# Kernel optimization log

Hardware: AMD Instinct MI355X
Metric: run time of the kernel (lower is better)

Reference implementation:

```python
import jax, jax.numpy as jnp
import numpy as np

B, NF, FD = 2048, 64, 32   # batch, n_features, feature_dim
S = NF // 2                # n_sites
D, OD = 32, 32             # bond_dim, out_dim


def setup_inputs() -> dict:
    key = jax.random.key(0)
    k1, k2, k3, k4 = jax.random.split(key, 4)
    sc = 1.0 / np.sqrt(FD * D)
    x = jax.random.normal(k1, (B, NF, FD), dtype=jnp.float32)
    L = jax.random.normal(k2, (S, FD, D, D), dtype=jnp.float32) * sc
    R = jax.random.normal(k3, (S, FD, D, D), dtype=jnp.float32) * sc
    O = jax.random.normal(k4, (S, D, D, OD), dtype=jnp.float32) * sc
    bias = jnp.zeros((S, OD), dtype=jnp.float32)
    return {"x": x, "L": L, "R": R, "O": O, "bias": bias}


def reference(x, L, R, O, bias):
    # x: [B, 2*S, FD] -> left/right features per site
    xL = x[:, 0::2, :]  # [B, S, FD]
    xR = x[:, 1::2, :]  # [B, S, FD]
    # feature -> bond matrices
    A = jnp.einsum('bsf,sfam->bsam', xL, L)   # [B, S, D, D]
    Bm = jnp.einsum('bsg,sgan->bsan', xR, R)  # [B, S, D, D]
    # contract shared bond leg a, then output tensor
    M = jnp.einsum('bsam,bsan->bsmn', A, Bm)  # [B, S, D, D]
    out = jnp.einsum('bsmn,smno->bso', M, O)  # [B, S, OD]
    return out + bias  # bias broadcast over batch; activation is None
```

## Files before the change

### kernel.cpp

```cpp
#include <hip/hip_runtime.h>
#include <hip/hip_bf16.h>

typedef __attribute__((ext_vector_type(4)))  _Float16 h4;
typedef __attribute__((ext_vector_type(8)))  _Float16 h8;
typedef __attribute__((ext_vector_type(4)))  float f32x4;
typedef __attribute__((ext_vector_type(16))) float f32x16;

__device__ __forceinline__ int sdecode(int sp) { return ((sp & 7) << 2) | (sp >> 3); }

__global__ __launch_bounds__(64) void conv_kernel(
    const float* __restrict__ Rg, const float* __restrict__ Og,
    _Float16* __restrict__ Rb, char* __restrict__ Opp)
{
    __shared__ float tile[32][33];
    const int bid = blockIdx.x;
    const int s = sdecode(bid & 31), q = (bid >> 5) & 31, which = bid >> 10;
    const int t = threadIdx.x, tl = t & 31, th = t >> 5;

    if (which == 0) {
        #pragma unroll
        for (int j = 0; j < 16; ++j) {
            int ar = 2*j + th;
            tile[tl][ar] = Rg[(((size_t)s*32 + q)*32 + ar)*32 + tl];
        }
        __syncthreads();
        _Float16* dst = Rb + ((size_t)s*32 + q)*1024;
        #pragma unroll
        for (int it = 0; it < 4; ++it) {
            int nr = it*8 + (t >> 3), a0 = (t & 7)*4;
            h4 w;
            #pragma unroll
            for (int k = 0; k < 4; ++k) w[k] = (_Float16)tile[nr][a0 + k];
            *(h4*)(dst + nr*32 + a0) = w;
        }
    } else {
        #pragma unroll
        for (int j = 0; j < 16; ++j) {
            int nr = 2*j + th;
            tile[tl][nr] = Og[(((size_t)s*32 + q)*32 + nr)*32 + tl];
        }
        __syncthreads();
        char* dst = Opp + (size_t)s*65536 + q*2048;
        int o = t & 31, cq = t >> 5;
        #pragma unroll
        for (int it = 0; it < 2; ++it) {
            int c = it*2 + cq;
            h8 w;
            #pragma unroll
            for (int k = 0; k < 8; ++k) w[k] = (_Float16)tile[o][c*8 + k];
            *(h8*)(dst + c*512 + o*16) = w;
        }
    }
}

__global__ __launch_bounds__(256, 2) void tmake_kernel(
    const float* __restrict__ Lg, const _Float16* __restrict__ Rb,
    const char* __restrict__ Opp, char* __restrict__ Tp)
{
    __shared__ __align__(16) char Wl[65536];
    const int bid = blockIdx.x;
    const int s = sdecode(bid & 31), f = bid >> 5;
    const int t = threadIdx.x, wid = t >> 6, l = t & 63;
    const int llo = l & 15, lhi = l >> 4;

    const float* Lsf = Lg + ((size_t)s*32 + f)*1024;
    h8 bfr[2];
    #pragma unroll
    for (int mt = 0; mt < 2; ++mt)
        #pragma unroll
        for (int j = 0; j < 8; ++j)
            bfr[mt][j] = (_Float16)Lsf[(8*lhi + j)*32 + mt*16 + llo];

    const _Float16* Rbs = Rb + (size_t)s*32768;

    #pragma unroll 4
    for (int nt = 0; nt < 16; ++nt) {
        int gnb = (wid*16 + nt)*16;
        h8 af = *(const h8*)(Rbs + (gnb + llo)*32 + 8*lhi);
        int g = gnb >> 5;
        int nbase = (gnb & 31) + 4*lhi;
        #pragma unroll
        for (int mt = 0; mt < 2; ++mt) {
            f32x4 d = __builtin_amdgcn_mfma_f32_16x16x32_f16(af, bfr[mt], (f32x4)(0.f), 0, 0, 0);
            int m = mt*16 + llo;
            h4 w;
            #pragma unroll
            for (int r = 0; r < 4; ++r) w[r] = (_Float16)d[r];
            int byte = (g*2048 + m*64 + nbase*2) ^ ((((g & 7) ^ (m & 7))) << 4);
            *(h4*)(Wl + byte) = w;
        }
    }
    __syncthreads();

    const int ot = wid & 1, kq = wid >> 1;
    const int orow = ot*16 + llo;
    const char* Opps = Opp + (size_t)s*65536;
    f32x4 acc0 = (f32x4)(0.f), acc1 = (f32x4)(0.f);
    #pragma unroll 4
    for (int ksl = 0; ksl < 16; ++ksl) {
        int ks = kq*16 + ksl;
        h8 bf = *(const h8*)(Opps + (ks*4 + lhi)*512 + orow*16);
        {
            int grow = llo;
            int byte = (grow*2048 + ks*64 + lhi*16) ^ ((((grow & 7) ^ (ks & 7))) << 4);
            h8 af = *(const h8*)(Wl + byte);
            acc0 = __builtin_amdgcn_mfma_f32_16x16x32_f16(af, bf, acc0, 0, 0, 0);
        }
        {
            int grow = 16 + llo;
            int byte = (grow*2048 + ks*64 + lhi*16) ^ ((((grow & 7) ^ (ks & 7))) << 4);
            h8 af = *(const h8*)(Wl + byte);
            acc1 = __builtin_amdgcn_mfma_f32_16x16x32_f16(af, bf, acc1, 0, 0, 0);
        }
    }
    __syncthreads();
    if (kq == 1) {
        *(f32x4*)(Wl + ((ot*2 + 0)*64 + l)*16) = acc0;
        *(f32x4*)(Wl + ((ot*2 + 1)*64 + l)*16) = acc1;
    }
    __syncthreads();
    if (kq == 0) {
        acc0 += *(const f32x4*)(Wl + ((ot*2 + 0)*64 + l)*16);
        acc1 += *(const f32x4*)(Wl + ((ot*2 + 1)*64 + l)*16);
        char* Tps = Tp + (size_t)s*65536;
        h4 w0, w1;
        #pragma unroll
        for (int r = 0; r < 4; ++r) { w0[r] = (_Float16)acc0[r]; w1[r] = (_Float16)acc1[r]; }
        *(h4*)(Tps + (f*2 + 0)*1024 + orow*32 + lhi*8) = w0;
        *(h4*)(Tps + (f*2 + 1)*1024 + orow*32 + lhi*8) = w1;
    }
}

__global__ __launch_bounds__(256, 2) void main_kernel(
    const float* __restrict__ x, const char* __restrict__ Tp,
    const float* __restrict__ bias, float* __restrict__ out)
{
    __shared__ __align__(16) char Tl[65536];

    const int bid = blockIdx.x;
    const int s = sdecode(bid & 31);
    const int b0 = (bid >> 5) * 128;
    const int t = threadIdx.x, wid = t >> 6, l = t & 63;
    const int lo5 = l & 31, hi = l >> 5;

    const char* Tps = Tp + (size_t)s*65536;

    uint4 tv[8];
    #pragma unroll
    for (int i = 0; i < 8; ++i)
        tv[i] = *(const uint4*)(Tps + (i*256 + t)*16);

    const float* xrow = x + (size_t)(b0 + wid*32 + lo5)*2048 + s*64;
    float4 xlv[8];
    #pragma unroll
    for (int i = 0; i < 8; ++i) xlv[i] = *(const float4*)(xrow + i*4);
    const float* xrp = xrow + 32 + hi*8;
    float4 xr00 = *(const float4*)(xrp);
    float4 xr01 = *(const float4*)(xrp + 4);
    float4 xr10 = *(const float4*)(xrp + 16);
    float4 xr11 = *(const float4*)(xrp + 20);

    #pragma unroll
    for (int i = 0; i < 8; ++i)
        *(uint4*)(Tl + (i*256 + t)*16) = tv[i];
    #pragma unroll
    for (int i = 0; i < 8; ++i)
        tv[i] = *(const uint4*)(Tps + ((i + 8)*256 + t)*16);

    h4 xlh[8];
    #pragma unroll
    for (int i = 0; i < 8; ++i) {
        xlh[i][0] = (_Float16)xlv[i].x; xlh[i][1] = (_Float16)xlv[i].y;
        xlh[i][2] = (_Float16)xlv[i].z; xlh[i][3] = (_Float16)xlv[i].w;
    }
    h8 xr_a, xr_b;
    xr_a[0] = (_Float16)xr00.x; xr_a[1] = (_Float16)xr00.y;
    xr_a[2] = (_Float16)xr00.z; xr_a[3] = (_Float16)xr00.w;
    xr_a[4] = (_Float16)xr01.x; xr_a[5] = (_Float16)xr01.y;
    xr_a[6] = (_Float16)xr01.z; xr_a[7] = (_Float16)xr01.w;
    xr_b[0] = (_Float16)xr10.x; xr_b[1] = (_Float16)xr10.y;
    xr_b[2] = (_Float16)xr10.z; xr_b[3] = (_Float16)xr10.w;
    xr_b[4] = (_Float16)xr11.x; xr_b[5] = (_Float16)xr11.y;
    xr_b[6] = (_Float16)xr11.z; xr_b[7] = (_Float16)xr11.w;

    #pragma unroll
    for (int i = 0; i < 8; ++i)
        *(uint4*)(Tl + ((i + 8)*256 + t)*16) = tv[i];
    __syncthreads();

    f32x16 acc_e = (f32x16)(0.f), acc_o = (f32x16)(0.f);
    #pragma unroll
    for (int ksl = 0; ksl < 64; ++ksl) {
        h8 bf = *(const h8*)(Tl + ksl*1024 + lo5*32 + hi*16);
        _Float16 xs = xlh[ksl >> 3][(ksl >> 1) & 3];
        if (ksl & 1) {
            h8 z = xr_b * xs;
            acc_o = __builtin_amdgcn_mfma_f32_32x32x16_f16(z, bf, acc_o, 0, 0, 0);
        } else {
            h8 z = xr_a * xs;
            acc_e = __builtin_amdgcn_mfma_f32_32x32x16_f16(z, bf, acc_e, 0, 0, 0);
        }
    }
    f32x16 acc = acc_e + acc_o;

    __syncthreads();
    #pragma unroll
    for (int r = 0; r < 16; ++r) {
        int row = (r & 3) + 8*(r >> 2) + 4*hi;
        *(float*)(Tl + wid*4096 + row*128 + lo5*4) = acc[r];
    }
    __syncthreads();

    const float* bias_s = bias + s*32;
    #pragma unroll
    for (int i = 0; i < 4; ++i) {
        int u = i*256 + t;
        int row = u >> 3, colq = u & 7;
        f32x4 v = *(const f32x4*)(Tl + u*16);
        f32x4 bv = *(const f32x4*)(bias_s + colq*4);
        *(f32x4*)(out + (size_t)(b0 + row)*1024 + s*32 + colq*4) = v + bv;
    }
}

extern "C" void kernel_launch(void* const* d_in, const int* in_sizes, int n_in,
                              void* d_out, int out_size, void* d_ws, size_t ws_size,
                              hipStream_t stream) {
    const float* x    = (const float*)d_in[0];
    const float* L    = (const float*)d_in[1];
    const float* R    = (const float*)d_in[2];
    const float* O    = (const float*)d_in[3];
    const float* bias = (const float*)d_in[4];
    float* out = (float*)d_out;

    _Float16* Rb  = (_Float16*)d_ws;
    char*     Opp = (char*)d_ws + 2097152;
    char*     Tp  = (char*)d_ws + 4194304;

    conv_kernel<<<dim3(2048), 64, 0, stream>>>(R, O, Rb, Opp);
    tmake_kernel<<<dim3(1024), 256, 0, stream>>>(L, Rb, Opp, Tp);
    main_kernel<<<dim3(512), 256, 0, stream>>>(x, Tp, bias, out);
}
```

Before: 28.90 us.

## Stream T fragments from global into register ring, drop LDS staging in main kernel

```diff
diff --git a/kernel.cpp b/kernel.cpp
--- a/kernel.cpp
+++ b/kernel.cpp
@@ -131,26 +131,20 @@
     }
 }
 
-__global__ __launch_bounds__(256, 2) void main_kernel(
+__global__ __launch_bounds__(64, 4) void main_kernel(
     const float* __restrict__ x, const char* __restrict__ Tp,
     const float* __restrict__ bias, float* __restrict__ out)
 {
-    __shared__ __align__(16) char Tl[65536];
-
     const int bid = blockIdx.x;
-    const int s = sdecode(bid & 31);
-    const int b0 = (bid >> 5) * 128;
-    const int t = threadIdx.x, wid = t >> 6, l = t & 63;
-    const int lo5 = l & 31, hi = l >> 5;
+    const int s = bid & 31;
+    const int b0 = (bid >> 5) * 32;
+    const int t = threadIdx.x;
+    const int lo5 = t & 31, hi = t >> 5;
 
     const char* Tps = Tp + (size_t)s*65536;
-
-    uint4 tv[8];
-    #pragma unroll
-    for (int i = 0; i < 8; ++i)
-        tv[i] = *(const uint4*)(Tps + (i*256 + t)*16);
-
-    const float* xrow = x + (size_t)(b0 + wid*32 + lo5)*2048 + s*64;
+    const char* Tbase = Tps + lo5*32 + hi*16;
+
+    const float* xrow = x + (size_t)(b0 + lo5)*2048 + s*64;
     float4 xlv[8];
     #pragma unroll
     for (int i = 0; i < 8; ++i) xlv[i] = *(const float4*)(xrow + i*4);
@@ -160,12 +154,10 @@
     float4 xr10 = *(const float4*)(xrp + 16);
     float4 xr11 = *(const float4*)(xrp + 20);
 
+    h8 ring[8];
     #pragma unroll
     for (int i = 0; i < 8; ++i)
-        *(uint4*)(Tl + (i*256 + t)*16) = tv[i];
-    #pragma unroll
-    for (int i = 0; i < 8; ++i)
-        tv[i] = *(const uint4*)(Tps + ((i + 8)*256 + t)*16);
+        ring[i] = *(const h8*)(Tbase + i*1024);
 
     h4 xlh[8];
     #pragma unroll
@@ -183,15 +175,12 @@
     xr_b[4] = (_Float16)xr11.x; xr_b[5] = (_Float16)xr11.y;
     xr_b[6] = (_Float16)xr11.z; xr_b[7] = (_Float16)xr11.w;
 
-    #pragma unroll
-    for (int i = 0; i < 8; ++i)
-        *(uint4*)(Tl + ((i + 8)*256 + t)*16) = tv[i];
-    __syncthreads();
-
     f32x16 acc_e = (f32x16)(0.f), acc_o = (f32x16)(0.f);
     #pragma unroll
     for (int ksl = 0; ksl < 64; ++ksl) {
-        h8 bf = *(const h8*)(Tl + ksl*1024 + lo5*32 + hi*16);
+        h8 bf = ring[ksl & 7];
+        if (ksl < 56)
+            ring[ksl & 7] = *(const h8*)(Tbase + (ksl + 8)*1024);
         _Float16 xs = xlh[ksl >> 3][(ksl >> 1) & 3];
         if (ksl & 1) {
             h8 z = xr_b * xs;
@@ -203,22 +192,11 @@
     }
     f32x16 acc = acc_e + acc_o;
 
-    __syncthreads();
+    const float bv = bias[s*32 + lo5];
     #pragma unroll
     for (int r = 0; r < 16; ++r) {
         int row = (r & 3) + 8*(r >> 2) + 4*hi;
-        *(float*)(Tl + wid*4096 + row*128 + lo5*4) = acc[r];
-    }
-    __syncthreads();
-
-    const float* bias_s = bias + s*32;
-    #pragma unroll
-    for (int i = 0; i < 4; ++i) {
-        int u = i*256 + t;
-        int row = u >> 3, colq = u & 7;
-        f32x4 v = *(const f32x4*)(Tl + u*16);
-        f32x4 bv = *(const f32x4*)(bias_s + colq*4);
-        *(f32x4*)(out + (size_t)(b0 + row)*1024 + s*32 + colq*4) = v + bv;
+        out[(size_t)(b0 + row)*1024 + s*32 + lo5] = acc[r] + bv;
     }
 }
 
@@ -238,5 +216,5 @@
 
     conv_kernel<<<dim3(2048), 64, 0, stream>>>(R, O, Rb, Opp);
     tmake_kernel<<<dim3(1024), 256, 0, stream>>>(L, Rb, Opp, Tp);
-    main_kernel<<<dim3(512), 256, 0, stream>>>(x, Tp, bias, out);
-}
+    main_kernel<<<dim3(2048), 64, 0, stream>>>(x, Tp, bias, out);
+}
```

Result: slower. 37.77 us (+30.7%).

## Fuse three kernels into one persistent kernel with per-site global barriers

Applied to the files above, without the earlier changes.

```diff
diff --git a/kernel.cpp b/kernel.cpp
--- a/kernel.cpp
+++ b/kernel.cpp
@@ -5,152 +5,159 @@
 typedef __attribute__((ext_vector_type(8)))  _Float16 h8;
 typedef __attribute__((ext_vector_type(4)))  float f32x4;
 typedef __attribute__((ext_vector_type(16))) float f32x16;
+typedef __attribute__((ext_vector_type(4)))  unsigned int u32x4;
 
 __device__ __forceinline__ int sdecode(int sp) { return ((sp & 7) << 2) | (sp >> 3); }
 
-__global__ __launch_bounds__(64) void conv_kernel(
+__global__ __launch_bounds__(256, 2) void fused_kernel(
+    const float* __restrict__ x, const float* __restrict__ Lg,
     const float* __restrict__ Rg, const float* __restrict__ Og,
-    _Float16* __restrict__ Rb, char* __restrict__ Opp)
+    const float* __restrict__ bias, float* __restrict__ out,
+    _Float16* __restrict__ Rb, char* __restrict__ Opp, char* __restrict__ Tp,
+    unsigned* __restrict__ bar)
 {
-    __shared__ float tile[32][33];
+    __shared__ __align__(16) char smem[65536];
+
     const int bid = blockIdx.x;
-    const int s = sdecode(bid & 31), q = (bid >> 5) & 31, which = bid >> 10;
-    const int t = threadIdx.x, tl = t & 31, th = t >> 5;
-
-    if (which == 0) {
-        #pragma unroll
-        for (int j = 0; j < 16; ++j) {
-            int ar = 2*j + th;
-            tile[tl][ar] = Rg[(((size_t)s*32 + q)*32 + ar)*32 + tl];
-        }
-        __syncthreads();
-        _Float16* dst = Rb + ((size_t)s*32 + q)*1024;
-        #pragma unroll
-        for (int it = 0; it < 4; ++it) {
-            int nr = it*8 + (t >> 3), a0 = (t & 7)*4;
-            h4 w;
-            #pragma unroll
-            for (int k = 0; k < 4; ++k) w[k] = (_Float16)tile[nr][a0 + k];
-            *(h4*)(dst + nr*32 + a0) = w;
-        }
-    } else {
-        #pragma unroll
-        for (int j = 0; j < 16; ++j) {
-            int nr = 2*j + th;
-            tile[tl][nr] = Og[(((size_t)s*32 + q)*32 + nr)*32 + tl];
-        }
-        __syncthreads();
-        char* dst = Opp + (size_t)s*65536 + q*2048;
-        int o = t & 31, cq = t >> 5;
+    const int sp = bid & 31, m = bid >> 5;
+    const int s = sdecode(sp);
+    const int t = threadIdx.x, wid = t >> 6, l = t & 63;
+
+    unsigned* cnt1 = bar + sp*64;
+    unsigned* cnt2 = bar + sp*64 + 32;
+
+    {
+        const int which = wid >> 1, q = 2*m + (wid & 1);
+        float (*tile)[33] = (float (*)[33])(smem + wid*4352);
+        const int tl = l & 31, th = l >> 5;
+
+        if (which == 0) {
+            #pragma unroll
+            for (int j = 0; j < 16; ++j) {
+                int ar = 2*j + th;
+                tile[tl][ar] = Rg[(((size_t)s*32 + q)*32 + ar)*32 + tl];
+            }
+        } else {
+            #pragma unroll
+            for (int j = 0; j < 16; ++j) {
+                int nr = 2*j + th;
+                tile[tl][nr] = Og[(((size_t)s*32 + q)*32 + nr)*32 + tl];
+            }
+        }
+        __syncthreads();
+        if (which == 0) {
+            _Float16* dst = Rb + ((size_t)s*32 + q)*1024;
+            #pragma unroll
+            for (int it = 0; it < 4; ++it) {
+                int nr = it*8 + (l >> 3), a0 = (l & 7)*4;
+                h4 w;
+                #pragma unroll
+                for (int k = 0; k < 4; ++k) w[k] = (_Float16)tile[nr][a0 + k];
+                *(h4*)(dst + nr*32 + a0) = w;
+            }
+        } else {
+            char* dst = Opp + (size_t)s*65536 + q*2048;
+            int o = l & 31, cq = l >> 5;
+            #pragma unroll
+            for (int it = 0; it < 2; ++it) {
+                int c = it*2 + cq;
+                h8 w;
+                #pragma unroll
+                for (int k = 0; k < 8; ++k) w[k] = (_Float16)tile[o][c*8 + k];
+                *(h8*)(dst + c*512 + o*16) = w;
+            }
+        }
+    }
+    asm volatile("s_waitcnt vmcnt(0) lgkmcnt(0)" ::: "memory");
+    __syncthreads();
+    if (t == 0) {
+        atomicAdd(cnt1, 1u);
+        while (__hip_atomic_load(cnt1, __ATOMIC_RELAXED, __HIP_MEMORY_SCOPE_AGENT) < 16u)
+            __builtin_amdgcn_s_sleep(16);
+    }
+    __syncthreads();
+
+    {
+        const int llo = l & 15, lhi = l >> 4;
+        const int ot = wid & 1, kq = wid >> 1;
+        const int orow = ot*16 + llo;
+        const _Float16* Rbs = Rb + (size_t)s*32768;
+        const char* Opps = Opp + (size_t)s*65536;
+        char* Wl = smem;
+
         #pragma unroll
         for (int it = 0; it < 2; ++it) {
-            int c = it*2 + cq;
-            h8 w;
-            #pragma unroll
-            for (int k = 0; k < 8; ++k) w[k] = (_Float16)tile[o][c*8 + k];
-            *(h8*)(dst + c*512 + o*16) = w;
-        }
-    }
-}
-
-__global__ __launch_bounds__(256, 2) void tmake_kernel(
-    const float* __restrict__ Lg, const _Float16* __restrict__ Rb,
-    const char* __restrict__ Opp, char* __restrict__ Tp)
-{
-    __shared__ __align__(16) char Wl[65536];
-    const int bid = blockIdx.x;
-    const int s = sdecode(bid & 31), f = bid >> 5;
-    const int t = threadIdx.x, wid = t >> 6, l = t & 63;
-    const int llo = l & 15, lhi = l >> 4;
-
-    const float* Lsf = Lg + ((size_t)s*32 + f)*1024;
-    h8 bfr[2];
-    #pragma unroll
-    for (int mt = 0; mt < 2; ++mt)
-        #pragma unroll
-        for (int j = 0; j < 8; ++j)
-            bfr[mt][j] = (_Float16)Lsf[(8*lhi + j)*32 + mt*16 + llo];
-
-    const _Float16* Rbs = Rb + (size_t)s*32768;
-
-    #pragma unroll 4
-    for (int nt = 0; nt < 16; ++nt) {
-        int gnb = (wid*16 + nt)*16;
-        h8 af = *(const h8*)(Rbs + (gnb + llo)*32 + 8*lhi);
-        int g = gnb >> 5;
-        int nbase = (gnb & 31) + 4*lhi;
-        #pragma unroll
-        for (int mt = 0; mt < 2; ++mt) {
-            f32x4 d = __builtin_amdgcn_mfma_f32_16x16x32_f16(af, bfr[mt], (f32x4)(0.f), 0, 0, 0);
-            int m = mt*16 + llo;
-            h4 w;
-            #pragma unroll
-            for (int r = 0; r < 4; ++r) w[r] = (_Float16)d[r];
-            int byte = (g*2048 + m*64 + nbase*2) ^ ((((g & 7) ^ (m & 7))) << 4);
-            *(h4*)(Wl + byte) = w;
-        }
-    }
-    __syncthreads();
-
-    const int ot = wid & 1, kq = wid >> 1;
-    const int orow = ot*16 + llo;
-    const char* Opps = Opp + (size_t)s*65536;
-    f32x4 acc0 = (f32x4)(0.f), acc1 = (f32x4)(0.f);
-    #pragma unroll 4
-    for (int ksl = 0; ksl < 16; ++ksl) {
-        int ks = kq*16 + ksl;
-        h8 bf = *(const h8*)(Opps + (ks*4 + lhi)*512 + orow*16);
-        {
-            int grow = llo;
-            int byte = (grow*2048 + ks*64 + lhi*16) ^ ((((grow & 7) ^ (ks & 7))) << 4);
-            h8 af = *(const h8*)(Wl + byte);
-            acc0 = __builtin_amdgcn_mfma_f32_16x16x32_f16(af, bf, acc0, 0, 0, 0);
-        }
-        {
-            int grow = 16 + llo;
-            int byte = (grow*2048 + ks*64 + lhi*16) ^ ((((grow & 7) ^ (ks & 7))) << 4);
-            h8 af = *(const h8*)(Wl + byte);
-            acc1 = __builtin_amdgcn_mfma_f32_16x16x32_f16(af, bf, acc1, 0, 0, 0);
-        }
-    }
-    __syncthreads();
-    if (kq == 1) {
-        *(f32x4*)(Wl + ((ot*2 + 0)*64 + l)*16) = acc0;
-        *(f32x4*)(Wl + ((ot*2 + 1)*64 + l)*16) = acc1;
-    }
-    __syncthreads();
-    if (kq == 0) {
-        acc0 += *(const f32x4*)(Wl + ((ot*2 + 0)*64 + l)*16);
-        acc1 += *(const f32x4*)(Wl + ((ot*2 + 1)*64 + l)*16);
-        char* Tps = Tp + (size_t)s*65536;
-        h4 w0, w1;
-        #pragma unroll
-        for (int r = 0; r < 4; ++r) { w0[r] = (_Float16)acc0[r]; w1[r] = (_Float16)acc1[r]; }
-        *(h4*)(Tps + (f*2 + 0)*1024 + orow*32 + lhi*8) = w0;
-        *(h4*)(Tps + (f*2 + 1)*1024 + orow*32 + lhi*8) = w1;
-    }
-}
-
-__global__ __launch_bounds__(256, 2) void main_kernel(
-    const float* __restrict__ x, const char* __restrict__ Tp,
-    const float* __restrict__ bias, float* __restrict__ out)
-{
-    __shared__ __align__(16) char Tl[65536];
-
-    const int bid = blockIdx.x;
-    const int s = sdecode(bid & 31);
-    const int b0 = (bid >> 5) * 128;
-    const int t = threadIdx.x, wid = t >> 6, l = t & 63;
+            const int f = 2*m + it;
+            if (it) __syncthreads();
+
+            const float* Lsf = Lg + ((size_t)s*32 + f)*1024;
+            h8 bfr[2];
+            #pragma unroll
+            for (int mt = 0; mt < 2; ++mt)
+                #pragma unroll
+                for (int j = 0; j < 8; ++j)
+                    bfr[mt][j] = (_Float16)Lsf[(8*lhi + j)*32 + mt*16 + llo];
+
+            #pragma unroll 4
+            for (int nt = 0; nt < 16; ++nt) {
+                int gnb = (wid*16 + nt)*16;
+                h8 af = *(const h8*)(Rbs + (gnb + llo)*32 + 8*lhi);
+                int g = gnb >> 5;
+                int nbase = (gnb & 31) + 4*lhi;
+                #pragma unroll
+                for (int mt = 0; mt < 2; ++mt) {
+                    f32x4 d = __builtin_amdgcn_mfma_f32_16x16x32_f16(af, bfr[mt], (f32x4)(0.f), 0, 0, 0);
+                    int mm = mt*16 + llo;
+                    h4 w;
+                    #pragma unroll
+                    for (int r = 0; r < 4; ++r) w[r] = (_Float16)d[r];
+                    int byte = (g*2048 + mm*64 + nbase*2) ^ ((((g & 7) ^ (mm & 7))) << 4);
+                    *(h4*)(Wl + byte) = w;
+                }
+            }
+            __syncthreads();
+
+            f32x4 acc0 = (f32x4)(0.f), acc1 = (f32x4)(0.f);
+            #pragma unroll 4
+            for (int ksl = 0; ksl < 16; ++ksl) {
+                int ks = kq*16 + ksl;
+                h8 bf = *(const h8*)(Opps + (ks*4 + lhi)*512 + orow*16);
+                {
+                    int grow = llo;
+                    int byte = (grow*2048 + ks*64 + lhi*16) ^ ((((grow & 7) ^ (ks & 7))) << 4);
+                    h8 af = *(const h8*)(Wl + byte);
+                    acc0 = __builtin_amdgcn_mfma_f32_16x16x32_f16(af, bf, acc0, 0, 0, 0);
+                }
+                {
+                    int grow = 16 + llo;
+                    int byte = (grow*2048 + ks*64 + lhi*16) ^ ((((grow & 7) ^ (ks & 7))) << 4);
+                    h8 af = *(const h8*)(Wl + byte);
+                    acc1 = __builtin_amdgcn_mfma_f32_16x16x32_f16(af, bf, acc1, 0, 0, 0);
+                }
+            }
+            __syncthreads();
+            if (kq == 1) {
+                *(f32x4*)(Wl + ((ot*2 + 0)*64 + l)*16) = acc0;
+                *(f32x4*)(Wl + ((ot*2 + 1)*64 + l)*16) = acc1;
+            }
+            __syncthreads();
+            if (kq == 0) {
+                acc0 += *(const f32x4*)(Wl + ((ot*2 + 0)*64 + l)*16);
+                acc1 += *(const f32x4*)(Wl + ((ot*2 + 1)*64 + l)*16);
+                char* Tps = Tp + (size_t)s*65536;
+                h4 w0, w1;
+                #pragma unroll
+                for (int r = 0; r < 4; ++r) { w0[r] = (_Float16)acc0[r]; w1[r] = (_Float16)acc1[r]; }
+                *(h4*)(Tps + (f*2 + 0)*1024 + orow*32 + lhi*8) = w0;
+                *(h4*)(Tps + (f*2 + 1)*1024 + orow*32 + lhi*8) = w1;
+            }
+        }
+    }
+
     const int lo5 = l & 31, hi = l >> 5;
-
-    const char* Tps = Tp + (size_t)s*65536;
-
-    uint4 tv[8];
-    #pragma unroll
-    for (int i = 0; i < 8; ++i)
-        tv[i] = *(const uint4*)(Tps + (i*256 + t)*16);
-
+    const int b0 = m * 128;
     const float* xrow = x + (size_t)(b0 + wid*32 + lo5)*2048 + s*64;
+    asm volatile("" ::: "memory");
     float4 xlv[8];
     #pragma unroll
     for (int i = 0; i < 8; ++i) xlv[i] = *(const float4*)(xrow + i*4);
@@ -160,65 +167,83 @@
     float4 xr10 = *(const float4*)(xrp + 16);
     float4 xr11 = *(const float4*)(xrp + 20);
 
-    #pragma unroll
-    for (int i = 0; i < 8; ++i)
-        *(uint4*)(Tl + (i*256 + t)*16) = tv[i];
-    #pragma unroll
-    for (int i = 0; i < 8; ++i)
-        tv[i] = *(const uint4*)(Tps + ((i + 8)*256 + t)*16);
-
-    h4 xlh[8];
-    #pragma unroll
-    for (int i = 0; i < 8; ++i) {
-        xlh[i][0] = (_Float16)xlv[i].x; xlh[i][1] = (_Float16)xlv[i].y;
-        xlh[i][2] = (_Float16)xlv[i].z; xlh[i][3] = (_Float16)xlv[i].w;
-    }
-    h8 xr_a, xr_b;
-    xr_a[0] = (_Float16)xr00.x; xr_a[1] = (_Float16)xr00.y;
-    xr_a[2] = (_Float16)xr00.z; xr_a[3] = (_Float16)xr00.w;
-    xr_a[4] = (_Float16)xr01.x; xr_a[5] = (_Float16)xr01.y;
-    xr_a[6] = (_Float16)xr01.z; xr_a[7] = (_Float16)xr01.w;
-    xr_b[0] = (_Float16)xr10.x; xr_b[1] = (_Float16)xr10.y;
-    xr_b[2] = (_Float16)xr10.z; xr_b[3] = (_Float16)xr10.w;
-    xr_b[4] = (_Float16)xr11.x; xr_b[5] = (_Float16)xr11.y;
-    xr_b[6] = (_Float16)xr11.z; xr_b[7] = (_Float16)xr11.w;
-
-    #pragma unroll
-    for (int i = 0; i < 8; ++i)
-        *(uint4*)(Tl + ((i + 8)*256 + t)*16) = tv[i];
-    __syncthreads();
-
-    f32x16 acc_e = (f32x16)(0.f), acc_o = (f32x16)(0.f);
-    #pragma unroll
-    for (int ksl = 0; ksl < 64; ++ksl) {
-        h8 bf = *(const h8*)(Tl + ksl*1024 + lo5*32 + hi*16);
-        _Float16 xs = xlh[ksl >> 3][(ksl >> 1) & 3];
-        if (ksl & 1) {
-            h8 z = xr_b * xs;
-            acc_o = __builtin_amdgcn_mfma_f32_32x32x16_f16(z, bf, acc_o, 0, 0, 0);
-        } else {
-            h8 z = xr_a * xs;
-            acc_e = __builtin_amdgcn_mfma_f32_32x32x16_f16(z, bf, acc_e, 0, 0, 0);
-        }
-    }
-    f32x16 acc = acc_e + acc_o;
-
-    __syncthreads();
-    #pragma unroll
-    for (int r = 0; r < 16; ++r) {
-        int row = (r & 3) + 8*(r >> 2) + 4*hi;
-        *(float*)(Tl + wid*4096 + row*128 + lo5*4) = acc[r];
-    }
-    __syncthreads();
-
-    const float* bias_s = bias + s*32;
-    #pragma unroll
-    for (int i = 0; i < 4; ++i) {
-        int u = i*256 + t;
-        int row = u >> 3, colq = u & 7;
-        f32x4 v = *(const f32x4*)(Tl + u*16);
-        f32x4 bv = *(const f32x4*)(bias_s + colq*4);
-        *(f32x4*)(out + (size_t)(b0 + row)*1024 + s*32 + colq*4) = v + bv;
+    asm volatile("s_waitcnt vmcnt(12) lgkmcnt(0)" ::: "memory");
+    __syncthreads();
+    if (t == 0) {
+        atomicAdd(cnt2, 1u);
+        while (__hip_atomic_load(cnt2, __ATOMIC_RELAXED, __HIP_MEMORY_SCOPE_AGENT) < 16u)
+            __builtin_amdgcn_s_sleep(16);
+    }
+    __syncthreads();
+
+    {
+        char* Tl = smem;
+        const char* Tps = Tp + (size_t)s*65536;
+
+        u32x4 tv[8];
+        #pragma unroll
+        for (int i = 0; i < 8; ++i)
+            tv[i] = *(const u32x4*)(Tps + (i*256 + t)*16);
+        #pragma unroll
+        for (int i = 0; i < 8; ++i)
+            *(u32x4*)(Tl + (i*256 + t)*16) = tv[i];
+        #pragma unroll
+        for (int i = 0; i < 8; ++i)
+            tv[i] = *(const u32x4*)(Tps + ((i + 8)*256 + t)*16);
+
+        h4 xlh[8];
+        #pragma unroll
+        for (int i = 0; i < 8; ++i) {
+            xlh[i][0] = (_Float16)xlv[i].x; xlh[i][1] = (_Float16)xlv[i].y;
+            xlh[i][2] = (_Float16)xlv[i].z; xlh[i][3] = (_Float16)xlv[i].w;
+        }
+        h8 xr_a, xr_b;
+        xr_a[0] = (_Float16)xr00.x; xr_a[1] = (_Float16)xr00.y;
+        xr_a[2] = (_Float16)xr00.z; xr_a[3] = (_Float16)xr00.w;
+        xr_a[4] = (_Float16)xr01.x; xr_a[5] = (_Float16)xr01.y;
+        xr_a[6] = (_Float16)xr01.z; xr_a[7] = (_Float16)xr01.w;
+        xr_b[0] = (_Float16)xr10.x; xr_b[1] = (_Float16)xr10.y;
+        xr_b[2] = (_Float16)xr10.z; xr_b[3] = (_Float16)xr10.w;
+        xr_b[4] = (_Float16)xr11.x; xr_b[5] = (_Float16)xr11.y;
+        xr_b[6] = (_Float16)xr11.z; xr_b[7] = (_Float16)xr11.w;
+
+        #pragma unroll
+        for (int i = 0; i < 8; ++i)
+            *(u32x4*)(Tl + ((i + 8)*256 + t)*16) = tv[i];
+        __syncthreads();
+
+        f32x16 acc_e = (f32x16)(0.f), acc_o = (f32x16)(0.f);
+        #pragma unroll
+        for (int ksl = 0; ksl < 64; ++ksl) {
+            h8 bf = *(const h8*)(Tl + ksl*1024 + lo5*32 + hi*16);
+            _Float16 xs = xlh[ksl >> 3][(ksl >> 1) & 3];
+            if (ksl & 1) {
+                h8 z = xr_b * xs;
+                acc_o = __builtin_amdgcn_mfma_f32_32x32x16_f16(z, bf, acc_o, 0, 0, 0);
+            } else {
+                h8 z = xr_a * xs;
+                acc_e = __builtin_amdgcn_mfma_f32_32x32x16_f16(z, bf, acc_e, 0, 0, 0);
+            }
+        }
+        f32x16 acc = acc_e + acc_o;
+
+        __syncthreads();
+        #pragma unroll
+        for (int r = 0; r < 16; ++r) {
+            int row = (r & 3) + 8*(r >> 2) + 4*hi;
+            *(float*)(Tl + wid*4096 + row*128 + lo5*4) = acc[r];
+        }
+        __syncthreads();
+
+        const float* bias_s = bias + s*32;
+        #pragma unroll
+        for (int i = 0; i < 4; ++i) {
+            int u = i*256 + t;
+            int row = u >> 3, colq = u & 7;
+            f32x4 v = *(const f32x4*)(Tl + u*16);
+            f32x4 bv = *(const f32x4*)(bias_s + colq*4);
+            *(f32x4*)(out + (size_t)(b0 + row)*1024 + s*32 + colq*4) = v + bv;
+        }
     }
 }
 
@@ -235,8 +260,9 @@
     _Float16* Rb  = (_Float16*)d_ws;
     char*     Opp = (char*)d_ws + 2097152;
     char*     Tp  = (char*)d_ws + 4194304;
-
-    conv_kernel<<<dim3(2048), 64, 0, stream>>>(R, O, Rb, Opp);
-    tmake_kernel<<<dim3(1024), 256, 0, stream>>>(L, Rb, Opp, Tp);
-    main_kernel<<<dim3(512), 256, 0, stream>>>(x, Tp, bias, out);
+    unsigned* bar = (unsigned*)((char*)d_ws + 6291456);
+
+    hipMemsetAsync(bar, 0, 8192, stream);
+    fused_kernel<<<dim3(512), dim3(256), 0, stream>>>(x, L, R, O, bias, out,
+                                                      Rb, Opp, Tp, bar);
 }
```

After: 32.99 us. 1.14x slower.
